# Kernel tuning notes

Measured on AMD Instinct MI355X. Metric: run time of the kernel, lower is better.

Reference implementation:

```python
import jax, jax.numpy as jnp
import numpy as np

DIM = 64
HID = 64      # hidden_dim
BATCH = 16384


def setup_inputs() -> dict:
    key = jax.random.key(0)
    ks = jax.random.split(key, 11)
    s = 0.05
    x = jax.random.normal(ks[0], (BATCH, DIM), dtype=jnp.float32)
    # network 0: Linear(1,H) -> ReLU -> Linear(H,2)
    w0 = jax.random.normal(ks[1], (1, HID), dtype=jnp.float32) * s
    b0 = jax.random.normal(ks[2], (HID,), dtype=jnp.float32) * s
    v0 = jax.random.normal(ks[3], (HID, 2), dtype=jnp.float32) * s
    c0 = jax.random.normal(ks[4], (2,), dtype=jnp.float32) * s
    # networks 1..DIM-1: Linear(i,H) -> ReLU -> Linear(H,H) -> ReLU -> Linear(H,2)
    # first-layer weights padded to full width DIM; columns >= i are masked out in reference().
    W1 = jax.random.normal(ks[5], (DIM - 1, DIM, HID), dtype=jnp.float32) * s
    B1 = jax.random.normal(ks[6], (DIM - 1, HID), dtype=jnp.float32) * s
    W2 = jax.random.normal(ks[7], (DIM - 1, HID, HID), dtype=jnp.float32) * s
    B2 = jax.random.normal(ks[8], (DIM - 1, HID), dtype=jnp.float32) * s
    W3 = jax.random.normal(ks[9], (DIM - 1, HID, 2), dtype=jnp.float32) * s
    B3 = jax.random.normal(ks[10], (DIM - 1, 2), dtype=jnp.float32) * s
    return {"x": x, "w0": w0, "b0": b0, "v0": v0, "c0": c0,
            "W1": W1, "B1": B1, "W2": W2, "B2": B2, "W3": W3, "B3": B3}


def reference(x, w0, b0, v0, c0, W1, B1, W2, B2, W3, B3):
    B, dim = x.shape
    # mask[i, j] = 1 if j < (i+1): network i+1 sees x[:, :i+1] prefix of width i+1... actually width i+1? No:
    # network index k (k = 1..dim-1) sees x[:, :k]. Row i of the stacks corresponds to k = i+1,
    # so valid input columns are j < i+1.
    mask = (jnp.arange(dim)[None, :] <= jnpp_dummy) if False else (jnp.arange(dim)[None, :] < (jnp.arange(1, dim)[:, None]))
    mask = mask.astype(x.dtype)                      # [dim-1, dim]
    W1m = W1 * mask[:, :, None]                      # zero out padded input columns
    h1 = jax.nn.relu(jnp.einsum('bd,idh->bih', x, W1m) + B1)   # [B, dim-1, H]
    h2 = jax.nn.relu(jnp.einsum('bih,ihg->big', h1, W2) + B2)  # [B, dim-1, H]
    out = jnp.einsum('big,igo->bio', h2, W3) + B3               # [B, dim-1, 2]
    # network 0 receives a constant ones input -> output is constant across the batch
    h0 = jax.nn.relu(w0[0] + b0)                     # [H]
    out0 = h0 @ v0 + c0                              # [2]
    out0 = jnp.broadcast_to(out0[None, None, :], (B, 1, 2))
    full = jnp.concatenate([out0, out], axis=1)      # [B, dim, 2]
    scales = jnp.clip(full[..., 0], -5.0, 5.0)
    translations = full[..., 1]
    return scales, translations

jnp_dummy = None
```

## Files before the change

kernel.cpp:

```cpp
#include <hip/hip_runtime.h>
#include <hip/hip_bf16.h>

#define BATCH 16384

typedef __attribute__((ext_vector_type(8))) short short8;
typedef __attribute__((ext_vector_type(4))) short short4v;
typedef __attribute__((ext_vector_type(2))) short sshort2;
typedef __attribute__((ext_vector_type(8))) unsigned short ushort8;
typedef __attribute__((ext_vector_type(4))) unsigned short ushort4v;
typedef __attribute__((ext_vector_type(4))) float float4v;

#define FR_A1      0u
#define FR_A2      516096u
#define FR_A3      1032192u
#define FR_SIZE    1161216u
#define XBF_SIZE   2097152u

__device__ __forceinline__ unsigned int packbf2(float a, float b) {
#if __has_builtin(__builtin_amdgcn_cvt_pk_bf16_f32)
    typedef __attribute__((ext_vector_type(2))) __bf16 bf2_t;
    union { bf2_t h; unsigned int u; } v;
    v.h = __builtin_amdgcn_cvt_pk_bf16_f32(a, b);
    return v.u;
#else
    union { __hip_bfloat162 h; unsigned int u; } v;
    v.h = __float22bfloat162_rn(make_float2(a, b));
    return v.u;
#endif
}
__device__ __forceinline__ unsigned int relu_pk(unsigned int u) {
#if __has_builtin(__builtin_elementwise_max)
    union { sshort2 s; unsigned int w; } v; v.w = u;
    v.s = __builtin_elementwise_max(v.s, (sshort2)0);
    return v.w;
#else
    unsigned int lo = (u & 0x8000u) ? 0u : (u & 0xFFFFu);
    unsigned int hi = (u & 0x80000000u) ? 0u : (u & 0xFFFF0000u);
    return lo | hi;
#endif
}
__device__ __forceinline__ unsigned int cvt_relu(float a, float b) {
    return relu_pk(packbf2(a, b));
}
__device__ __forceinline__ unsigned short f2bf(float a) {
    union { __hip_bfloat16 h; unsigned short u; } v;
    v.h = __float2bfloat16(a);
    return v.u;
}

__global__ __launch_bounds__(256) void setup_kernel(
    const float* __restrict__ x,
    const float* __restrict__ W1,
    const float* __restrict__ W2,
    const float* __restrict__ W3,
    char* __restrict__ frag,
    char* __restrict__ xbf)
{
    const int b = blockIdx.x;
    const int t = threadIdx.x;

    if (b >= 63) {
        const int idx = (b - 63) * 256 + t;
        const float* xp = x + (size_t)idx * 16;
        char* dst = xbf + (size_t)idx * 32;
        #pragma unroll
        for (int h = 0; h < 2; ++h) {
            float4v f0 = *(const float4v*)(xp + h * 8);
            float4v f1 = *(const float4v*)(xp + h * 8 + 4);
            union { ushort8 s; unsigned int u[4]; } p;
            p.u[0] = packbf2(f0[0], f0[1]);
            p.u[1] = packbf2(f0[2], f0[3]);
            p.u[2] = packbf2(f1[0], f1[1]);
            p.u[3] = packbf2(f1[2], f1[3]);
            *(ushort8*)(dst + h * 16) = p.s;
        }
        return;
    }

    const int kn   = b;
    const int net  = kn + 1;
    const int lane = t & 63;
    const int grp  = t >> 6;
    const int lq   = lane & 15;
    const int quad = lane >> 4;

    {
        const int h = lq + 16 * grp;
        ushort8 a10, a11;
        #pragma unroll
        for (int j = 0; j < 8; ++j) {
            const int d0 = quad * 8 + j;
            const int d1 = d0 + 32;
            a10[j] = (d0 < net) ? f2bf(W1[kn * 4096 + d0 * 64 + h]) : (unsigned short)0;
            a11[j] = (d1 < net) ? f2bf(W1[kn * 4096 + d1 * 64 + h]) : (unsigned short)0;
        }
        char* dst = frag + FR_A1 + kn * 8192 + grp * 2048 + lane * 32;
        *(ushort8*)(dst)      = a10;
        *(ushort8*)(dst + 16) = a11;
    }

    {
        const int g = lq + 16 * grp;
        #pragma unroll
        for (int th = 0; th < 4; ++th) {
            ushort4v v;
            #pragma unroll
            for (int i = 0; i < 4; ++i) {
                const int h = quad * 4 + 16 * th + i;
                v[i] = f2bf(W2[kn * 4096 + h * 64 + g]);
            }
            *(ushort4v*)(frag + FR_A2 + kn * 8192 + lane * 128 + grp * 32 + th * 8) = v;
        }
    }

    {
        ushort4v v;
        #pragma unroll
        for (int i = 0; i < 4; ++i) {
            const int g = quad * 4 + 16 * grp + i;
            v[i] = (lq < 2) ? f2bf(W3[kn * 128 + g * 2 + lq]) : (unsigned short)0;
        }
        *(ushort4v*)(frag + FR_A3 + kn * 2048 + lane * 32 + grp * 8) = v;
    }
}

template <bool XBF>
__global__ __launch_bounds__(256, 3) void arnet_main4(
    const float* __restrict__ x,
    const char* __restrict__ xbf,
    const char* __restrict__ frag,
    const float* __restrict__ w0, const float* __restrict__ b0,
    const float* __restrict__ v0, const float* __restrict__ c0,
    const float* __restrict__ B1, const float* __restrict__ B2,
    const float* __restrict__ B3,
    float* __restrict__ out)
{
    const int bi    = blockIdx.x;
    const int chunk = bi & 63;
    const int g     = bi >> 6;
    const int t     = threadIdx.x;

    const int lane = t & 63;
    const int w    = t >> 6;
    const int lq   = lane & 15;
    const int quad = lane >> 4;

    __shared__ float sOut[2][256][5];

    const int rowbase = chunk * 256 + w * 64;

    short8 xf[4][2];
    #pragma unroll
    for (int tm = 0; tm < 4; ++tm) {
        if (XBF) {
            const char* base = xbf + (size_t)(rowbase + 16 * tm + lq) * 128 + quad * 16;
            xf[tm][0] = *(const short8*)(base);
            xf[tm][1] = *(const short8*)(base + 64);
        } else {
            const float* xr = x + (size_t)(rowbase + 16 * tm + lq) * 64 + quad * 8;
            #pragma unroll
            for (int half = 0; half < 2; ++half) {
                float4v f0 = *(const float4v*)(xr + 32 * half);
                float4v f1 = *(const float4v*)(xr + 32 * half + 4);
                union { short8 s; unsigned int u[4]; } p;
                p.u[0] = packbf2(f0[0], f0[1]);
                p.u[1] = packbf2(f0[2], f0[3]);
                p.u[2] = packbf2(f1[0], f1[1]);
                p.u[3] = packbf2(f1[2], f1[3]);
                xf[tm][half] = p.s;
            }
        }
    }

    #pragma unroll 1
    for (int idx = 0; idx < 4; ++idx) {
        const int net = g * 4 + idx;

        if (net == 0) {
            float s = 0.f, tr = 0.f;
            #pragma unroll 8
            for (int j = 0; j < 64; ++j) {
                float h = fmaxf(w0[j] + b0[j], 0.f);
                s  += h * v0[2 * j];
                tr += h * v0[2 * j + 1];
            }
            s += c0[0];
            tr += c0[1];
            s = fminf(fmaxf(s, -5.f), 5.f);
            sOut[0][t][0] = s;
            sOut[1][t][0] = tr;
            continue;
        }

        const int kn = net - 1;
        const char* pA1 = frag + FR_A1 + kn * 8192 + lane * 32;
        const char* pA2 = frag + FR_A2 + kn * 8192 + lane * 128;
        const char* pA3 = frag + FR_A3 + kn * 2048 + lane * 32;

        float4v acc2[4][4];
        #pragma unroll
        for (int th = 0; th < 4; ++th) {
            short8 a10 = *(const short8*)(pA1 + th * 2048);
            short8 a11 = *(const short8*)(pA1 + th * 2048 + 16);
            float4v bias1 = *(const float4v*)(B1 + kn * 64 + quad * 4 + 16 * th);
            short4v bf1[4];
            #pragma unroll
            for (int tm = 0; tm < 4; ++tm) {
                float4v acc1;
                acc1 = __builtin_amdgcn_mfma_f32_16x16x32_bf16(a10, xf[tm][0], bias1, 0, 0, 0);
                acc1 = __builtin_amdgcn_mfma_f32_16x16x32_bf16(a11, xf[tm][1], acc1, 0, 0, 0);
                union { short4v s; unsigned int u[2]; } pk;
                pk.u[0] = cvt_relu(acc1[0], acc1[1]);
                pk.u[1] = cvt_relu(acc1[2], acc1[3]);
                bf1[tm] = pk.s;
            }
            if (th == 0) {
                #pragma unroll
                for (int tg = 0; tg < 4; ++tg) {
                    short4v a2 = *(const short4v*)(pA2 + tg * 32);
                    float4v bias2 = *(const float4v*)(B2 + kn * 64 + quad * 4 + 16 * tg);
                    #pragma unroll
                    for (int tm = 0; tm < 4; ++tm)
                        acc2[tg][tm] = __builtin_amdgcn_mfma_f32_16x16x16bf16_1k(a2, bf1[tm], bias2, 0, 0, 0);
                }
            } else {
                #pragma unroll
                for (int tg = 0; tg < 4; ++tg) {
                    short4v a2 = *(const short4v*)(pA2 + tg * 32 + th * 8);
                    #pragma unroll
                    for (int tm = 0; tm < 4; ++tm)
                        acc2[tg][tm] = __builtin_amdgcn_mfma_f32_16x16x16bf16_1k(a2, bf1[tm], acc2[tg][tm], 0, 0, 0);
                }
            }
        }

        float4v c3v;
        c3v[0] = B3[kn * 2]; c3v[1] = B3[kn * 2 + 1]; c3v[2] = 0.f; c3v[3] = 0.f;
        float4v acc3[4];
        #pragma unroll
        for (int tg = 0; tg < 4; ++tg) {
            short4v a3 = *(const short4v*)(pA3 + tg * 8);
            #pragma unroll
            for (int tm = 0; tm < 4; ++tm) {
                union { short4v s; unsigned int u[2]; } pk;
                pk.u[0] = cvt_relu(acc2[tg][tm][0], acc2[tg][tm][1]);
                pk.u[1] = cvt_relu(acc2[tg][tm][2], acc2[tg][tm][3]);
                acc3[tm] = __builtin_amdgcn_mfma_f32_16x16x16bf16_1k(a3, pk.s, (tg == 0) ? c3v : acc3[tm], 0, 0, 0);
            }
        }

        if (quad == 0) {
            #pragma unroll
            for (int tm = 0; tm < 4; ++tm) {
                const int lr = w * 64 + 16 * tm + lq;
                sOut[0][lr][idx] = fminf(fmaxf(acc3[tm][0], -5.f), 5.f);
                sOut[1][lr][idx] = acc3[tm][1];
            }
        }
    }

    __syncthreads();

    {
        const int row = t;
        const size_t grow = (size_t)chunk * 256 + row;
        #pragma unroll
        for (int o = 0; o < 2; ++o) {
            float4v v4;
            #pragma unroll
            for (int j = 0; j < 4; ++j) v4[j] = sOut[o][row][j];
            float* dst = out + ((size_t)o * BATCH + grow) * 64 + 4 * g;
            *(float4v*)(dst) = v4;
        }
    }
}

#define WPAD 72
__global__ __launch_bounds__(256) void arnet_fallback(
    const float* __restrict__ x, const float* __restrict__ w0, const float* __restrict__ b0,
    const float* __restrict__ v0, const float* __restrict__ c0,
    const float* __restrict__ W1, const float* __restrict__ B1,
    const float* __restrict__ W2, const float* __restrict__ B2,
    const float* __restrict__ W3, const float* __restrict__ B3,
    float* __restrict__ out)
{
    const int bi = blockIdx.x;
    const int net = bi >> 5;
    const int tile = bi & 31;
    const int t = threadIdx.x;
    if (net == 0) {
        float s = 0.f, tr = 0.f;
        for (int j = 0; j < 64; ++j) {
            float h = fmaxf(w0[j] + b0[j], 0.f);
            s += h * v0[2 * j]; tr += h * v0[2 * j + 1];
        }
        s += c0[0]; tr += c0[1];
        s = fminf(fmaxf(s, -5.f), 5.f);
        const size_t r0 = (size_t)tile * 512;
        out[(r0 + t) * 64] = s; out[(size_t)BATCH * 64 + (r0 + t) * 64] = tr;
        out[(r0 + 256 + t) * 64] = s; out[(size_t)BATCH * 64 + (r0 + 256 + t) * 64] = tr;
        return;
    }
    __shared__ unsigned short sW1T[64 * WPAD];
    __shared__ unsigned short sW2T[64 * WPAD];
    __shared__ unsigned short sW3T[2 * 64];
    __shared__ float sB1[64];
    __shared__ float sB2[64];
    const int kn = net - 1;
    {
        const int hb = (t & 15) * 4, jb = (t >> 4) * 4;
        const float* src1 = W1 + kn * 4096;
        const float* src2 = W2 + kn * 4096;
        float4v a[4], b[4];
        for (int jj = 0; jj < 4; ++jj) {
            a[jj] = *(const float4v*)(src1 + (jb + jj) * 64 + hb);
            if (jb + jj >= net) a[jj] = (float4v)0.f;
            b[jj] = *(const float4v*)(src2 + (jb + jj) * 64 + hb);
        }
        for (int hh = 0; hh < 4; ++hh) {
            ushort4v ra, rb;
            for (int jj = 0; jj < 4; ++jj) { ra[jj] = f2bf(a[jj][hh]); rb[jj] = f2bf(b[jj][hh]); }
            *(ushort4v*)(&sW1T[(hb + hh) * WPAD + jb]) = ra;
            *(ushort4v*)(&sW2T[(hb + hh) * WPAD + jb]) = rb;
        }
    }
    if (t < 64) {
        sW3T[t] = f2bf(W3[kn * 128 + t * 2]);
        sW3T[64 + t] = f2bf(W3[kn * 128 + t * 2 + 1]);
        sB1[t] = B1[kn * 64 + t];
        sB2[t] = B2[kn * 64 + t];
    }
    const float b30 = B3[kn * 2], b31 = B3[kn * 2 + 1];
    __syncthreads();
    const int lane = t & 63, w = t >> 6, lq = lane & 15, quad = lane >> 4;
    for (int pass = 0; pass < 2; ++pass) {
        const int rowbase = tile * 512 + pass * 256 + w * 64;
        short8 xf[4][2];
        for (int tm = 0; tm < 4; ++tm) {
            const float* xr = x + (size_t)(rowbase + 16 * tm + lq) * 64 + quad * 8;
            for (int half = 0; half < 2; ++half) {
                float4v f0 = *(const float4v*)(xr + 32 * half);
                float4v f1 = *(const float4v*)(xr + 32 * half + 4);
                union { short8 s; unsigned int u[4]; } p;
                p.u[0] = packbf2(f0[0], f0[1]); p.u[1] = packbf2(f0[2], f0[3]);
                p.u[2] = packbf2(f1[0], f1[1]); p.u[3] = packbf2(f1[2], f1[3]);
                xf[tm][half] = p.s;
            }
        }
        float4v acc2[4][4];
        for (int tg = 0; tg < 4; ++tg) {
            float4v bias2 = *(const float4v*)(&sB2[quad * 4 + 16 * tg]);
            for (int tm = 0; tm < 4; ++tm) acc2[tg][tm] = bias2;
        }
        for (int th = 0; th < 4; ++th) {
            float4v bias1 = *(const float4v*)(&sB1[quad * 4 + 16 * th]);
            short8 a10 = *(const short8*)(&sW1T[(lq + 16 * th) * WPAD + quad * 8]);
            short8 a11 = *(const short8*)(&sW1T[(lq + 16 * th) * WPAD + quad * 8 + 32]);
            float4v acc1[4];
            for (int tm = 0; tm < 4; ++tm) {
                acc1[tm] = bias1;
                acc1[tm] = __builtin_amdgcn_mfma_f32_16x16x32_bf16(a10, xf[tm][0], acc1[tm], 0, 0, 0);
                acc1[tm] = __builtin_amdgcn_mfma_f32_16x16x32_bf16(a11, xf[tm][1], acc1[tm], 0, 0, 0);
            }
            short4v bf1[4];
            for (int tm = 0; tm < 4; ++tm) {
                union { short4v s; unsigned int u[2]; } pk;
                pk.u[0] = cvt_relu(acc1[tm][0], acc1[tm][1]);
                pk.u[1] = cvt_relu(acc1[tm][2], acc1[tm][3]);
                bf1[tm] = pk.s;
            }
            for (int tg = 0; tg < 4; ++tg) {
                short4v a2 = *(const short4v*)(&sW2T[(lq + 16 * tg) * WPAD + quad * 4 + 16 * th]);
                for (int tm = 0; tm < 4; ++tm)
                    acc2[tg][tm] = __builtin_amdgcn_mfma_f32_16x16x16bf16_1k(a2, bf1[tm], acc2[tg][tm], 0, 0, 0);
            }
        }
        float4v acc3[4];
        for (int tm = 0; tm < 4; ++tm) { acc3[tm][0] = b30; acc3[tm][1] = b31; acc3[tm][2] = 0.f; acc3[tm][3] = 0.f; }
        for (int tg = 0; tg < 4; ++tg) {
            short4v a3 = (short4v)0;
            if (lq < 2) a3 = *(const short4v*)(&sW3T[lq * 64 + quad * 4 + 16 * tg]);
            for (int tm = 0; tm < 4; ++tm) {
                union { short4v s; unsigned int u[2]; } pk;
                pk.u[0] = cvt_relu(acc2[tg][tm][0], acc2[tg][tm][1]);
                pk.u[1] = cvt_relu(acc2[tg][tm][2], acc2[tg][tm][3]);
                acc3[tm] = __builtin_amdgcn_mfma_f32_16x16x16bf16_1k(a3, pk.s, acc3[tm], 0, 0, 0);
            }
        }
        if (quad == 0) {
            for (int tm = 0; tm < 4; ++tm) {
                const size_t r = (size_t)(rowbase + 16 * tm + lq);
                out[r * 64 + net] = fminf(fmaxf(acc3[tm][0], -5.f), 5.f);
                out[(size_t)BATCH * 64 + r * 64 + net] = acc3[tm][1];
            }
        }
    }
}

extern "C" void kernel_launch(void* const* d_in, const int* in_sizes, int n_in,
                              void* d_out, int out_size, void* d_ws, size_t ws_size,
                              hipStream_t stream) {
    const float* x  = (const float*)d_in[0];
    const float* w0 = (const float*)d_in[1];
    const float* b0 = (const float*)d_in[2];
    const float* v0 = (const float*)d_in[3];
    const float* c0 = (const float*)d_in[4];
    const float* W1 = (const float*)d_in[5];
    const float* B1 = (const float*)d_in[6];
    const float* W2 = (const float*)d_in[7];
    const float* B2 = (const float*)d_in[8];
    const float* W3 = (const float*)d_in[9];
    const float* B3 = (const float*)d_in[10];
    float* out = (float*)d_out;
    char* ws = (char*)d_ws;

    const dim3 blk(256);

    if (ws_size >= FR_SIZE + XBF_SIZE) {
        char* xbf = ws + FR_SIZE;
        setup_kernel<<<dim3(63 + 256), blk, 0, stream>>>(x, W1, W2, W3, ws, xbf);
        arnet_main4<true><<<dim3(1024), blk, 0, stream>>>(
            x, xbf, ws, w0, b0, v0, c0, B1, B2, B3, out);
    } else if (ws_size >= FR_SIZE) {
        setup_kernel<<<dim3(63), blk, 0, stream>>>(x, W1, W2, W3, ws, nullptr);
        arnet_main4<false><<<dim3(1024), blk, 0, stream>>>(
            x, nullptr, ws, w0, b0, v0, c0, B1, B2, B3, out);
    } else {
        arnet_fallback<<<dim3(64 * 32), blk, 0, stream>>>(
            x, w0, b0, v0, c0, W1, B1, W2, B2, W3, B3, out);
    }
}
```

Before: 121.9 us.

## Stage per-network weight fragments into LDS with double-buffered async loads

Repacks the per-network weight fragments and biases into one contiguous record per network, with a wave-friendly layout in global memory. The main kernel now copies each network's record into a double-buffered shared-memory tile using global_load_lds, prefetching the next network while the current one computes. The setup kernel also stages W1/W2 through shared memory so its transposing reads are coalesced. This cuts the redundant global/L2 fragment reads done by every wave. In exchange it adds about 38KB of LDS per block, which may lower occupancy, and a barrier per network iteration.

```diff
diff --git a/kernel.cpp b/kernel.cpp
--- a/kernel.cpp
+++ b/kernel.cpp
@@ -10,11 +10,14 @@
 typedef __attribute__((ext_vector_type(4))) unsigned short ushort4v;
 typedef __attribute__((ext_vector_type(4))) float float4v;
 
-#define FR_A1      0u
-#define FR_A2      516096u
-#define FR_A3      1032192u
-#define FR_SIZE    1161216u
+#define FR_STRIDE  18944u
+#define FR_SIZE    (63u * FR_STRIDE)
+#define OFF_A2     8192u
+#define OFF_A3     16384u
+#define OFF_B1     18432u
+#define OFF_B2     18688u
 #define XBF_SIZE   2097152u
+#define FR_ELEMS   1184
 
 __device__ __forceinline__ unsigned int packbf2(float a, float b) {
 #if __has_builtin(__builtin_amdgcn_cvt_pk_bf16_f32)
@@ -48,11 +51,20 @@
     return v.u;
 }
 
+__device__ __forceinline__ void gl_lds16(const char* gsrc, char* ldst) {
+    __builtin_amdgcn_global_load_lds(
+        (const __attribute__((address_space(1))) unsigned int*)gsrc,
+        (__attribute__((address_space(3))) unsigned int*)ldst,
+        16, 0, 0);
+}
+
 __global__ __launch_bounds__(256) void setup_kernel(
     const float* __restrict__ x,
     const float* __restrict__ W1,
     const float* __restrict__ W2,
     const float* __restrict__ W3,
+    const float* __restrict__ B1,
+    const float* __restrict__ B2,
     char* __restrict__ frag,
     char* __restrict__ xbf)
 {
@@ -77,6 +89,9 @@
         return;
     }
 
+    __shared__ float sW1[4096];
+    __shared__ float sW2[4096];
+
     const int kn   = b;
     const int net  = kn + 1;
     const int lane = t & 63;
@@ -85,16 +100,29 @@
     const int quad = lane >> 4;
 
     {
+        const float4v* s1 = (const float4v*)(W1 + kn * 4096);
+        const float4v* s2 = (const float4v*)(W2 + kn * 4096);
+        #pragma unroll
+        for (int i = 0; i < 4; ++i) {
+            ((float4v*)sW1)[i * 256 + t] = s1[i * 256 + t];
+            ((float4v*)sW2)[i * 256 + t] = s2[i * 256 + t];
+        }
+    }
+    __syncthreads();
+
+    char* base = frag + (size_t)kn * FR_STRIDE;
+
+    {
         const int h = lq + 16 * grp;
         ushort8 a10, a11;
         #pragma unroll
         for (int j = 0; j < 8; ++j) {
             const int d0 = quad * 8 + j;
             const int d1 = d0 + 32;
-            a10[j] = (d0 < net) ? f2bf(W1[kn * 4096 + d0 * 64 + h]) : (unsigned short)0;
-            a11[j] = (d1 < net) ? f2bf(W1[kn * 4096 + d1 * 64 + h]) : (unsigned short)0;
-        }
-        char* dst = frag + FR_A1 + kn * 8192 + grp * 2048 + lane * 32;
+            a10[j] = (d0 < net) ? f2bf(sW1[d0 * 64 + h]) : (unsigned short)0;
+            a11[j] = (d1 < net) ? f2bf(sW1[d1 * 64 + h]) : (unsigned short)0;
+        }
+        char* dst = base + grp * 2048 + lane * 32;
         *(ushort8*)(dst)      = a10;
         *(ushort8*)(dst + 16) = a11;
     }
@@ -107,9 +135,9 @@
             #pragma unroll
             for (int i = 0; i < 4; ++i) {
                 const int h = quad * 4 + 16 * th + i;
-                v[i] = f2bf(W2[kn * 4096 + h * 64 + g]);
-            }
-            *(ushort4v*)(frag + FR_A2 + kn * 8192 + lane * 128 + grp * 32 + th * 8) = v;
+                v[i] = f2bf(sW2[h * 64 + g]);
+            }
+            *(ushort4v*)(base + OFF_A2 + grp * 2048 + th * 512 + lane * 8) = v;
         }
     }
 
@@ -120,7 +148,12 @@
             const int g = quad * 4 + 16 * grp + i;
             v[i] = (lq < 2) ? f2bf(W3[kn * 128 + g * 2 + lq]) : (unsigned short)0;
         }
-        *(ushort4v*)(frag + FR_A3 + kn * 2048 + lane * 32 + grp * 8) = v;
+        *(ushort4v*)(base + OFF_A3 + grp * 512 + lane * 8) = v;
+    }
+
+    if (t < 64) {
+        *(float*)(base + OFF_B1 + t * 4) = B1[kn * 64 + t];
+        *(float*)(base + OFF_B2 + t * 4) = B2[kn * 64 + t];
     }
 }
 
@@ -131,7 +164,6 @@
     const char* __restrict__ frag,
     const float* __restrict__ w0, const float* __restrict__ b0,
     const float* __restrict__ v0, const float* __restrict__ c0,
-    const float* __restrict__ B1, const float* __restrict__ B2,
     const float* __restrict__ B3,
     float* __restrict__ out)
 {
@@ -145,6 +177,7 @@
     const int lq   = lane & 15;
     const int quad = lane >> 4;
 
+    __shared__ __align__(16) char sFrag[2][FR_STRIDE];
     __shared__ float sOut[2][256][5];
 
     const int rowbase = chunk * 256 + w * 64;
@@ -172,9 +205,26 @@
         }
     }
 
+    auto stage = [&](int net_, char* dstb) {
+        const char* src = frag + (size_t)(net_ - 1) * FR_STRIDE;
+        #pragma unroll
+        for (int i = 0; i < 5; ++i) {
+            const int e = i * 256 + t;
+            if (e < FR_ELEMS)
+                gl_lds16(src + e * 16, dstb + e * 16);
+        }
+    };
+
+    const int first = (g == 0) ? 1 : 0;
+    stage(g * 4 + first, sFrag[first & 1]);
+    __syncthreads();
+
     #pragma unroll 1
     for (int idx = 0; idx < 4; ++idx) {
         const int net = g * 4 + idx;
+
+        if (idx + 1 < 4 && idx + 1 > first)
+            stage(g * 4 + idx + 1, sFrag[(idx + 1) & 1]);
 
         if (net == 0) {
             float s = 0.f, tr = 0.f;
@@ -189,20 +239,24 @@
             s = fminf(fmaxf(s, -5.f), 5.f);
             sOut[0][t][0] = s;
             sOut[1][t][0] = tr;
+            __syncthreads();
             continue;
         }
 
         const int kn = net - 1;
-        const char* pA1 = frag + FR_A1 + kn * 8192 + lane * 32;
-        const char* pA2 = frag + FR_A2 + kn * 8192 + lane * 128;
-        const char* pA3 = frag + FR_A3 + kn * 2048 + lane * 32;
+        const char* sf  = sFrag[idx & 1];
+        const char* pA1 = sf + lane * 32;
+        const char* pA2 = sf + OFF_A2 + lane * 8;
+        const char* pA3 = sf + OFF_A3 + lane * 8;
+        const float* bB1 = (const float*)(sf + OFF_B1);
+        const float* bB2 = (const float*)(sf + OFF_B2);
 
         float4v acc2[4][4];
         #pragma unroll
         for (int th = 0; th < 4; ++th) {
             short8 a10 = *(const short8*)(pA1 + th * 2048);
             short8 a11 = *(const short8*)(pA1 + th * 2048 + 16);
-            float4v bias1 = *(const float4v*)(B1 + kn * 64 + quad * 4 + 16 * th);
+            float4v bias1 = *(const float4v*)(bB1 + quad * 4 + 16 * th);
             short4v bf1[4];
             #pragma unroll
             for (int tm = 0; tm < 4; ++tm) {
@@ -217,8 +271,8 @@
             if (th == 0) {
                 #pragma unroll
                 for (int tg = 0; tg < 4; ++tg) {
-                    short4v a2 = *(const short4v*)(pA2 + tg * 32);
-                    float4v bias2 = *(const float4v*)(B2 + kn * 64 + quad * 4 + 16 * tg);
+                    short4v a2 = *(const short4v*)(pA2 + tg * 2048);
+                    float4v bias2 = *(const float4v*)(bB2 + quad * 4 + 16 * tg);
                     #pragma unroll
                     for (int tm = 0; tm < 4; ++tm)
                         acc2[tg][tm] = __builtin_amdgcn_mfma_f32_16x16x16bf16_1k(a2, bf1[tm], bias2, 0, 0, 0);
@@ -226,7 +280,7 @@
             } else {
                 #pragma unroll
                 for (int tg = 0; tg < 4; ++tg) {
-                    short4v a2 = *(const short4v*)(pA2 + tg * 32 + th * 8);
+                    short4v a2 = *(const short4v*)(pA2 + tg * 2048 + th * 512);
                     #pragma unroll
                     for (int tm = 0; tm < 4; ++tm)
                         acc2[tg][tm] = __builtin_amdgcn_mfma_f32_16x16x16bf16_1k(a2, bf1[tm], acc2[tg][tm], 0, 0, 0);
@@ -239,7 +293,7 @@
         float4v acc3[4];
         #pragma unroll
         for (int tg = 0; tg < 4; ++tg) {
-            short4v a3 = *(const short4v*)(pA3 + tg * 8);
+            short4v a3 = *(const short4v*)(pA3 + tg * 512);
             #pragma unroll
             for (int tm = 0; tm < 4; ++tm) {
                 union { short4v s; unsigned int u[2]; } pk;
@@ -257,9 +311,8 @@
                 sOut[1][lr][idx] = acc3[tm][1];
             }
         }
-    }
-
-    __syncthreads();
+        __syncthreads();
+    }
 
     {
         const int row = t;
@@ -418,13 +471,13 @@
 
     if (ws_size >= FR_SIZE + XBF_SIZE) {
         char* xbf = ws + FR_SIZE;
-        setup_kernel<<<dim3(63 + 256), blk, 0, stream>>>(x, W1, W2, W3, ws, xbf);
+        setup_kernel<<<dim3(63 + 256), blk, 0, stream>>>(x, W1, W2, W3, B1, B2, ws, xbf);
         arnet_main4<true><<<dim3(1024), blk, 0, stream>>>(
-            x, xbf, ws, w0, b0, v0, c0, B1, B2, B3, out);
+            x, xbf, ws, w0, b0, v0, c0, B3, out);
     } else if (ws_size >= FR_SIZE) {
-        setup_kernel<<<dim3(63), blk, 0, stream>>>(x, W1, W2, W3, ws, nullptr);
+        setup_kernel<<<dim3(63), blk, 0, stream>>>(x, W1, W2, W3, B1, B2, ws, nullptr);
         arnet_main4<false><<<dim3(1024), blk, 0, stream>>>(
-            x, nullptr, ws, w0, b0, v0, c0, B1, B2, B3, out);
+            x, nullptr, ws, w0, b0, v0, c0, B3, out);
     } else {
         arnet_fallback<<<dim3(64 * 32), blk, 0, stream>>>(
             x, w0, b0, v0, c0, W1, B1, W2, B2, W3, B3, out);
```

Result: faster. 108.5 us (-11.0%).
